# Kernel tuning notes

Measured on AMD Instinct MI355X. Metric: run time of the kernel, lower is better.

Reference implementation:

```python
import jax, jax.numpy as jnp
import numpy as np

NORM_CONSTANT = 1.0
EPS = 1e-8

def setup_inputs() -> dict:
    key = jax.random.key(0)
    ks = jax.random.split(key, 8)
    bs, n, nf, hid = 16, 512, 7, 64
    return {
        "x": jax.random.normal(ks[0], (bs, n, 3), dtype=jnp.float32),
        "h": jax.random.normal(ks[1], (bs * n, nf), dtype=jnp.float32),
        "pose": jax.random.normal(ks[2], (bs * n, 3, 3), dtype=jnp.float32),
        "node_mask": jnp.ones((bs, n, 1), dtype=jnp.float32),
        "W1": jax.random.normal(ks[3], (nf, hid), dtype=jnp.float32) / np.sqrt(nf),
        "b1": jax.random.normal(ks[4], (hid,), dtype=jnp.float32) * 0.01,
        "W2": jax.random.normal(ks[5], (hid, 2), dtype=jnp.float32) / np.sqrt(hid),
        "b2": jax.random.normal(ks[6], (2,), dtype=jnp.float32) * 0.01,
    }


def reference(x, h, pose, node_mask, W1, b1, W2, b2):
    bs, n, _ = x.shape
    m = node_mask  # [bs, n, 1]
    # remove_mean_with_mask
    mean = jnp.sum(x * m, axis=1, keepdims=True) / jnp.sum(m, axis=1, keepdims=True)
    xc = (x - mean) * m  # [bs, n, 3]
    # coord2diff over fully-connected edges: row=i, col=j
    cd = xc[:, :, None, :] - xc[:, None, :, :]          # [bs, n, n, 3]
    radial = jnp.sum(cd * cd, axis=-1, keepdims=True)   # [bs, n, n, 1]
    cd = cd / (jnp.sqrt(radial + EPS) + NORM_CONSTANT)
    # pose transform: einsum('bijpk,bikm->bijpm', cd[...,None,:], pose.transpose(-1,-2))
    pose_b = pose.reshape(bs, n, 3, 3)
    tc = jnp.einsum('bijk,bimk->bijm', cd, pose_b)       # [bs, n, n, 3]
    # feature embedding MLP: Linear -> SiLU -> Linear
    he = jax.nn.silu(h @ W1 + b1) @ W2 + b2              # [bs*n, 2]
    he = he.reshape(bs, n, 2)
    # h_i gathers the row node (index i for all j), h_j the column node -> broadcasts
    hi = jnp.broadcast_to(he[:, :, None, :], (bs, n, n, 2))
    hj = jnp.broadcast_to(he[:, None, :, :], (bs, n, n, 2))
    edge_features = jnp.concatenate([radial, tc, hi, hj], axis=-1)  # [bs, n, n, 8]
    return edge_features
```

## Files before the change

kernel.cpp:

```cpp
#include <hip/hip_runtime.h>
#include <math.h>

#define BS 16
#define N 512
#define NF 7
#define HID 64

__global__ __launch_bounds__(256) void center_kernel(const float* __restrict__ x,
                                                     const float* __restrict__ mask,
                                                     float4* __restrict__ xcpad) {
    const int b = blockIdx.x;
    const int t = threadIdx.x;

    float lx[2], ly[2], lz[2], lm[2];
    float sx = 0.f, sy = 0.f, sz = 0.f, sm = 0.f;
    for (int k = 0; k < 2; ++k) {
        const int j = t + k * 256;
        const float* p = x + ((size_t)b * N + j) * 3;
        const float m = mask[(size_t)b * N + j];
        lx[k] = p[0]; ly[k] = p[1]; lz[k] = p[2]; lm[k] = m;
        sx += lx[k] * m; sy += ly[k] * m; sz += lz[k] * m; sm += m;
    }
    for (int off = 32; off > 0; off >>= 1) {
        sx += __shfl_down(sx, off, 64);
        sy += __shfl_down(sy, off, 64);
        sz += __shfl_down(sz, off, 64);
        sm += __shfl_down(sm, off, 64);
    }
    __shared__ float red[4][4];
    __shared__ float meanv[3];
    const int wave = t >> 6, lane = t & 63;
    if (lane == 0) { red[wave][0] = sx; red[wave][1] = sy; red[wave][2] = sz; red[wave][3] = sm; }
    __syncthreads();
    if (t == 0) {
        float tx = 0.f, ty = 0.f, tz = 0.f, tm = 0.f;
        for (int w = 0; w < 4; ++w) { tx += red[w][0]; ty += red[w][1]; tz += red[w][2]; tm += red[w][3]; }
        meanv[0] = tx / tm; meanv[1] = ty / tm; meanv[2] = tz / tm;
    }
    __syncthreads();
    const float mx = meanv[0], my = meanv[1], mz = meanv[2];
    for (int k = 0; k < 2; ++k) {
        const int j = t + k * 256;
        const float m = lm[k];
        xcpad[(size_t)b * N + j] =
            make_float4((lx[k] - mx) * m, (ly[k] - my) * m, (lz[k] - mz) * m, 0.f);
    }
}

__global__ __launch_bounds__(256) void mlp_kernel(const float* __restrict__ h,
                                                  const float* __restrict__ W1,
                                                  const float* __restrict__ b1,
                                                  const float* __restrict__ W2,
                                                  const float* __restrict__ b2,
                                                  float2* __restrict__ he) {
    __shared__ float sW1[NF * HID];
    __shared__ float sb1[HID];
    __shared__ float sW2[HID * 2];
    const int t = threadIdx.x;
    for (int idx = t; idx < NF * HID; idx += 256) sW1[idx] = W1[idx];
    if (t < HID) sb1[t] = b1[t];
    if (t < HID * 2) sW2[t] = W2[t];
    __syncthreads();

    const int node = blockIdx.x * 256 + t;
    float hv[NF];
    for (int j = 0; j < NF; ++j) hv[j] = h[(size_t)node * NF + j];
    float o0 = b2[0], o1 = b2[1];
    for (int k = 0; k < HID; ++k) {
        float a = sb1[k];
        for (int j = 0; j < NF; ++j) a += hv[j] * sW1[j * HID + k];
        const float s = a / (1.f + expf(-a));
        o0 += s * sW2[k * 2 + 0];
        o1 += s * sW2[k * 2 + 1];
    }
    he[node] = make_float2(o0, o1);
}

__global__ __launch_bounds__(256) void edge_kernel(const float4* __restrict__ xcpad,
                                                   const float2* __restrict__ he,
                                                   const float* __restrict__ pose,
                                                   float* __restrict__ out) {
    const int i = blockIdx.x;
    const int b = blockIdx.y;
    const int t = threadIdx.x;
    const int node_i = b * N + i;

    const float4 xi = xcpad[node_i];
    const float2 hi = he[node_i];
    const float* pp = pose + (size_t)node_i * 9;
    const float p00 = pp[0], p01 = pp[1], p02 = pp[2];
    const float p10 = pp[3], p11 = pp[4], p12 = pp[5];
    const float p20 = pp[6], p21 = pp[7], p22 = pp[8];

    const size_t outbase = (size_t)node_i * N * 8;
    for (int k = 0; k < 2; ++k) {
        const int j = t + k * 256;
        const float4 xj = xcpad[b * N + j];
        const float2 hj = he[b * N + j];
        const float c0 = xi.x - xj.x, c1 = xi.y - xj.y, c2 = xi.z - xj.z;
        const float r = c0 * c0 + c1 * c1 + c2 * c2;
        const float inv = 1.0f / (sqrtf(r + 1e-8f) + 1.0f);
        const float d0 = c0 * inv, d1 = c1 * inv, d2 = c2 * inv;
        const float t0 = p00 * d0 + p01 * d1 + p02 * d2;
        const float t1 = p10 * d0 + p11 * d1 + p12 * d2;
        const float t2 = p20 * d0 + p21 * d1 + p22 * d2;
        float4* o = (float4*)(out + outbase + (size_t)j * 8);
        o[0] = make_float4(r, t0, t1, t2);
        o[1] = make_float4(hi.x, hi.y, hj.x, hj.y);
    }
}

extern "C" void kernel_launch(void* const* d_in, const int* in_sizes, int n_in,
                              void* d_out, int out_size, void* d_ws, size_t ws_size,
                              hipStream_t stream) {
    const float* x    = (const float*)d_in[0];
    const float* h    = (const float*)d_in[1];
    const float* pose = (const float*)d_in[2];
    const float* mask = (const float*)d_in[3];
    const float* W1   = (const float*)d_in[4];
    const float* b1   = (const float*)d_in[5];
    const float* W2   = (const float*)d_in[6];
    const float* b2   = (const float*)d_in[7];
    float* out = (float*)d_out;

    float4* xcpad = (float4*)d_ws;
    float2* hebuf = (float2*)((char*)d_ws + (size_t)BS * N * 16);

    hipLaunchKernelGGL(center_kernel, dim3(BS), dim3(256), 0, stream, x, mask, xcpad);
    hipLaunchKernelGGL(mlp_kernel, dim3(BS * N / 256), dim3(256), 0, stream,
                       h, W1, b1, W2, b2, hebuf);
    hipLaunchKernelGGL(edge_kernel, dim3(N, BS), dim3(256), 0, stream,
                       xcpad, hebuf, pose, out);
}
```

Before: 162.7 us.

## Merge prep kernels and write edge output with coalesced nontemporal 16-byte stores

Merges the centering and MLP kernels into one launch, with blocks branching on blockIdx to pick their task, which removes one kernel launch. The edge kernel now has each thread write one 16-byte half of an edge record, so consecutive lanes write contiguous memory rather than two strided float4 stores per thread. Those stores use nontemporal hints to avoid polluting the cache with the large write-once output. In exchange, every edge is computed twice, once by each of its two threads, and each thread evaluates a branch on lane parity.

```diff
diff --git a/kernel.cpp b/kernel.cpp
--- a/kernel.cpp
+++ b/kernel.cpp
@@ -6,80 +6,82 @@
 #define NF 7
 #define HID 64
 
-__global__ __launch_bounds__(256) void center_kernel(const float* __restrict__ x,
-                                                     const float* __restrict__ mask,
-                                                     float4* __restrict__ xcpad) {
-    const int b = blockIdx.x;
+typedef float nfloat4 __attribute__((ext_vector_type(4)));
+
+__global__ __launch_bounds__(256) void prep_kernel(const float* __restrict__ x,
+                                                   const float* __restrict__ mask,
+                                                   const float* __restrict__ h,
+                                                   const float* __restrict__ W1,
+                                                   const float* __restrict__ b1,
+                                                   const float* __restrict__ W2,
+                                                   const float* __restrict__ b2,
+                                                   float4* __restrict__ xcpad,
+                                                   float2* __restrict__ he) {
     const int t = threadIdx.x;
 
-    float lx[2], ly[2], lz[2], lm[2];
-    float sx = 0.f, sy = 0.f, sz = 0.f, sm = 0.f;
-    for (int k = 0; k < 2; ++k) {
-        const int j = t + k * 256;
-        const float* p = x + ((size_t)b * N + j) * 3;
-        const float m = mask[(size_t)b * N + j];
-        lx[k] = p[0]; ly[k] = p[1]; lz[k] = p[2]; lm[k] = m;
-        sx += lx[k] * m; sy += ly[k] * m; sz += lz[k] * m; sm += m;
+    if (blockIdx.x < BS) {
+        const int b = blockIdx.x;
+        float lx[2], ly[2], lz[2], lm[2];
+        float sx = 0.f, sy = 0.f, sz = 0.f, sm = 0.f;
+        for (int k = 0; k < 2; ++k) {
+            const int j = t + k * 256;
+            const float* p = x + ((size_t)b * N + j) * 3;
+            const float m = mask[(size_t)b * N + j];
+            lx[k] = p[0]; ly[k] = p[1]; lz[k] = p[2]; lm[k] = m;
+            sx += lx[k] * m; sy += ly[k] * m; sz += lz[k] * m; sm += m;
+        }
+        for (int off = 32; off > 0; off >>= 1) {
+            sx += __shfl_down(sx, off, 64);
+            sy += __shfl_down(sy, off, 64);
+            sz += __shfl_down(sz, off, 64);
+            sm += __shfl_down(sm, off, 64);
+        }
+        __shared__ float red[4][4];
+        __shared__ float meanv[3];
+        const int wave = t >> 6, lane = t & 63;
+        if (lane == 0) { red[wave][0] = sx; red[wave][1] = sy; red[wave][2] = sz; red[wave][3] = sm; }
+        __syncthreads();
+        if (t == 0) {
+            float tx = 0.f, ty = 0.f, tz = 0.f, tm = 0.f;
+            for (int w = 0; w < 4; ++w) { tx += red[w][0]; ty += red[w][1]; tz += red[w][2]; tm += red[w][3]; }
+            meanv[0] = tx / tm; meanv[1] = ty / tm; meanv[2] = tz / tm;
+        }
+        __syncthreads();
+        const float mx = meanv[0], my = meanv[1], mz = meanv[2];
+        for (int k = 0; k < 2; ++k) {
+            const int j = t + k * 256;
+            const float m = lm[k];
+            xcpad[(size_t)b * N + j] =
+                make_float4((lx[k] - mx) * m, (ly[k] - my) * m, (lz[k] - mz) * m, 0.f);
+        }
+    } else {
+        __shared__ float sW1[NF * HID];
+        __shared__ float sb1[HID];
+        __shared__ float sW2[HID * 2];
+        for (int idx = t; idx < NF * HID; idx += 256) sW1[idx] = W1[idx];
+        if (t < HID) sb1[t] = b1[t];
+        if (t < HID * 2) sW2[t] = W2[t];
+        __syncthreads();
+
+        const int node = (blockIdx.x - BS) * 256 + t;
+        float hv[NF];
+        for (int j = 0; j < NF; ++j) hv[j] = h[(size_t)node * NF + j];
+        float o0 = b2[0], o1 = b2[1];
+        for (int k = 0; k < HID; ++k) {
+            float a = sb1[k];
+            for (int j = 0; j < NF; ++j) a += hv[j] * sW1[j * HID + k];
+            const float s = a / (1.f + expf(-a));
+            o0 += s * sW2[k * 2 + 0];
+            o1 += s * sW2[k * 2 + 1];
+        }
+        he[node] = make_float2(o0, o1);
     }
-    for (int off = 32; off > 0; off >>= 1) {
-        sx += __shfl_down(sx, off, 64);
-        sy += __shfl_down(sy, off, 64);
-        sz += __shfl_down(sz, off, 64);
-        sm += __shfl_down(sm, off, 64);
-    }
-    __shared__ float red[4][4];
-    __shared__ float meanv[3];
-    const int wave = t >> 6, lane = t & 63;
-    if (lane == 0) { red[wave][0] = sx; red[wave][1] = sy; red[wave][2] = sz; red[wave][3] = sm; }
-    __syncthreads();
-    if (t == 0) {
-        float tx = 0.f, ty = 0.f, tz = 0.f, tm = 0.f;
-        for (int w = 0; w < 4; ++w) { tx += red[w][0]; ty += red[w][1]; tz += red[w][2]; tm += red[w][3]; }
-        meanv[0] = tx / tm; meanv[1] = ty / tm; meanv[2] = tz / tm;
-    }
-    __syncthreads();
-    const float mx = meanv[0], my = meanv[1], mz = meanv[2];
-    for (int k = 0; k < 2; ++k) {
-        const int j = t + k * 256;
-        const float m = lm[k];
-        xcpad[(size_t)b * N + j] =
-            make_float4((lx[k] - mx) * m, (ly[k] - my) * m, (lz[k] - mz) * m, 0.f);
-    }
-}
-
-__global__ __launch_bounds__(256) void mlp_kernel(const float* __restrict__ h,
-                                                  const float* __restrict__ W1,
-                                                  const float* __restrict__ b1,
-                                                  const float* __restrict__ W2,
-                                                  const float* __restrict__ b2,
-                                                  float2* __restrict__ he) {
-    __shared__ float sW1[NF * HID];
-    __shared__ float sb1[HID];
-    __shared__ float sW2[HID * 2];
-    const int t = threadIdx.x;
-    for (int idx = t; idx < NF * HID; idx += 256) sW1[idx] = W1[idx];
-    if (t < HID) sb1[t] = b1[t];
-    if (t < HID * 2) sW2[t] = W2[t];
-    __syncthreads();
-
-    const int node = blockIdx.x * 256 + t;
-    float hv[NF];
-    for (int j = 0; j < NF; ++j) hv[j] = h[(size_t)node * NF + j];
-    float o0 = b2[0], o1 = b2[1];
-    for (int k = 0; k < HID; ++k) {
-        float a = sb1[k];
-        for (int j = 0; j < NF; ++j) a += hv[j] * sW1[j * HID + k];
-        const float s = a / (1.f + expf(-a));
-        o0 += s * sW2[k * 2 + 0];
-        o1 += s * sW2[k * 2 + 1];
-    }
-    he[node] = make_float2(o0, o1);
 }
 
 __global__ __launch_bounds__(256) void edge_kernel(const float4* __restrict__ xcpad,
                                                    const float2* __restrict__ he,
                                                    const float* __restrict__ pose,
-                                                   float* __restrict__ out) {
+                                                   nfloat4* __restrict__ out) {
     const int i = blockIdx.x;
     const int b = blockIdx.y;
     const int t = threadIdx.x;
@@ -92,9 +94,12 @@
     const float p10 = pp[3], p11 = pp[4], p12 = pp[5];
     const float p20 = pp[6], p21 = pp[7], p22 = pp[8];
 
-    const size_t outbase = (size_t)node_i * N * 8;
-    for (int k = 0; k < 2; ++k) {
-        const int j = t + k * 256;
+    nfloat4* __restrict__ orow = out + (size_t)node_i * N * 2;
+
+    #pragma unroll
+    for (int k = 0; k < 4; ++k) {
+        const int idx = k * 256 + t;
+        const int j = idx >> 1;
         const float4 xj = xcpad[b * N + j];
         const float2 hj = he[b * N + j];
         const float c0 = xi.x - xj.x, c1 = xi.y - xj.y, c2 = xi.z - xj.z;
@@ -104,9 +109,10 @@
         const float t0 = p00 * d0 + p01 * d1 + p02 * d2;
         const float t1 = p10 * d0 + p11 * d1 + p12 * d2;
         const float t2 = p20 * d0 + p21 * d1 + p22 * d2;
-        float4* o = (float4*)(out + outbase + (size_t)j * 8);
-        o[0] = make_float4(r, t0, t1, t2);
-        o[1] = make_float4(hi.x, hi.y, hj.x, hj.y);
+        nfloat4 v;
+        if (idx & 1) { v.x = hi.x; v.y = hi.y; v.z = hj.x; v.w = hj.y; }
+        else         { v.x = r;    v.y = t0;   v.z = t1;   v.w = t2;   }
+        __builtin_nontemporal_store(v, orow + idx);
     }
 }
 
@@ -121,14 +127,13 @@
     const float* b1   = (const float*)d_in[5];
     const float* W2   = (const float*)d_in[6];
     const float* b2   = (const float*)d_in[7];
-    float* out = (float*)d_out;
+    nfloat4* out = (nfloat4*)d_out;
 
     float4* xcpad = (float4*)d_ws;
     float2* hebuf = (float2*)((char*)d_ws + (size_t)BS * N * 16);
 
-    hipLaunchKernelGGL(center_kernel, dim3(BS), dim3(256), 0, stream, x, mask, xcpad);
-    hipLaunchKernelGGL(mlp_kernel, dim3(BS * N / 256), dim3(256), 0, stream,
-                       h, W1, b1, W2, b2, hebuf);
+    hipLaunchKernelGGL(prep_kernel, dim3(BS + BS * N / 256), dim3(256), 0, stream,
+                       x, mask, h, W1, b1, W2, b2, xcpad, hebuf);
     hipLaunchKernelGGL(edge_kernel, dim3(N, BS), dim3(256), 0, stream,
                        xcpad, hebuf, pose, out);
 }
```

After: 164.2 us. No clear change (+0.9%).
